# Optimization experiments

Hardware: AMD Instinct MI355X
Metric: run time of the kernel (lower is better)

## Reference

```python
import jax, jax.numpy as jnp
import numpy as np

B, H, S, D = 1, 16, 4096, 64
TEMPERATURE = 8.0          # sqrt(d_k)
WINDOW_SIZE = 256
HALF_WINDOW = WINDOW_SIZE // 2
NEG_INF = -1000000000.0


def setup_inputs() -> dict:
    key = jax.random.key(0)
    kq, kk, kv = jax.random.split(key, 3)
    q = jax.random.normal(kq, (B, H, S, D), dtype=jnp.float32)
    k = jax.random.normal(kk, (B, H, S, D), dtype=jnp.float32)
    v = jax.random.normal(kv, (B, H, S, D), dtype=jnp.float32)
    return {"q": q, "k": k, "v": v}


def reference(q, k, v):
    # q,k,v: [B,H,S,D]
    seq = q.shape[2]
    attn = jnp.einsum('bhqd,bhkd->bhqk', q, k) / TEMPERATURE  # [B,H,S,S]
    if seq > WINDOW_SIZE:
        idx = jnp.arange(seq)
        # torch loop: row i allows columns [i-half, i+half] inclusive
        win = jnp.abs(idx[:, None] - idx[None, :]) <= HALF_WINDOW  # [S,S]
        attn = jnp.where(win[None, None, :, :], attn, NEG_INF)
    attn = jax.nn.softmax(attn, axis=-1)  # dropout p=0 -> identity
    out = jnp.einsum('bhqk,bhkd->bhqd', attn, v)
    return (out, attn)
```

## Files before the change

### kernel.cpp

```cpp
#include <hip/hip_runtime.h>
#include <hip/hip_bf16.h>


typedef short bf16x8 __attribute__((ext_vector_type(8)));
typedef float f32x4  __attribute__((ext_vector_type(4)));
typedef unsigned int u32;
typedef unsigned short u16;

namespace {
constexpr int S = 4096, H = 16, Dh = 64, TRB = 64, HW = 128, NCH = 5;
constexpr int KP  = 72;
constexpr int NTILE = H * (S / TRB);
}

__device__ __forceinline__ u16 f2bf(float x) {
    u32 u = __float_as_uint(x);
    return (u16)((u + 0x7fffu + ((u >> 16) & 1u)) >> 16);
}
__device__ __forceinline__ float bf2f(u16 h) {
    return __uint_as_float(((u32)h) << 16);
}

__device__ __forceinline__ void bar_lds() {
    asm volatile("s_waitcnt lgkmcnt(0)" ::: "memory");
    __builtin_amdgcn_s_barrier();
    asm volatile("" ::: "memory");
}

__global__ __launch_bounds__(256)
void zfill(float* __restrict__ attn)
{
    constexpr size_t NF4     = (size_t)H * S * S / 4;
    constexpr size_t PER_BLK = NF4 / 256;
    f32x4* dst = (f32x4*)attn + (size_t)blockIdx.x * PER_BLK;
    const f32x4 z4 = {0.f, 0.f, 0.f, 0.f};
    for (size_t i = threadIdx.x; i < PER_BLK; i += 1024) {
        dst[i]       = z4;
        dst[i + 256] = z4;
        dst[i + 512] = z4;
        dst[i + 768] = z4;
    }
}

__global__ __launch_bounds__(256, 4)
void wattn(const float* __restrict__ q, const float* __restrict__ k,
           const float* __restrict__ v, float* __restrict__ out,
           float* __restrict__ attn)
{
    __shared__ __align__(16) u16 hbuf[4 * 64 * KP];
    __shared__ float inv_row[TRB];
    u16* kh_ = hbuf;
    u16* kl_ = hbuf + 64 * KP;
    u16* vt_ = hbuf + 2 * 64 * KP;
    u16* pc_ = hbuf + 3 * 64 * KP;

    const int tid  = threadIdx.x;
    const int wave = tid >> 6, lane = tid & 63;
    const int g = lane >> 4, m = lane & 15;

    int bx = blockIdx.x;
    bx = (bx & 7) * (NTILE / 8) + (bx >> 3);
    const int h  = bx >> 6;
    const int r0 = (bx & 63) * TRB;
    const int c0 = max(0, r0 - HW);
    const int c1 = min(S - 1, r0 + TRB - 1 + HW);
    const int c0q = c0 >> 2;

    const float* qp = q + ((size_t)h * S + r0) * Dh;
    const float* kp = k + (size_t)h * S * Dh;
    const float* vp = v + (size_t)h * S * Dh;
    float* arow = attn + ((size_t)h * S + r0) * S;

    bf16x8 aqh[2], aql[2];
    #pragma unroll
    for (int ks = 0; ks < 2; ++ks) {
        const float* qsrc = qp + (wave * 16 + m) * Dh + ks * 32 + g * 8;
        float4 t0 = *(const float4*)(qsrc);
        float4 t1 = *(const float4*)(qsrc + 4);
        float xs[8] = {t0.x, t0.y, t0.z, t0.w, t1.x, t1.y, t1.z, t1.w};
        #pragma unroll
        for (int i = 0; i < 8; ++i) {
            u16 hi = f2bf(xs[i]);
            aqh[ks][i] = (short)hi;
            aql[ks][i] = (short)f2bf(xs[i] - bf2f(hi));
        }
    }

    const int kcol = tid >> 2, kd = (tid & 3) * 16;
    const int vj = tid & 63, vd = (tid >> 6) * 16;

    float4 rk[4], rv[4];
    {
        const float* src = kp + (size_t)min(c0 + kcol, S - 1) * Dh + kd;
        #pragma unroll
        for (int i4 = 0; i4 < 4; ++i4) rk[i4] = *(const float4*)(src + i4 * 4);
    }
    {
        const float* src = vp + (size_t)min(c0 + vj, S - 1) * Dh + vd;
        #pragma unroll
        for (int i4 = 0; i4 < 4; ++i4) rv[i4] = *(const float4*)(src + i4 * 4);
    }

    float rs[4] = {0.f, 0.f, 0.f, 0.f};
    f32x4 oacc[4] = {{0.f,0.f,0.f,0.f},{0.f,0.f,0.f,0.f},
                     {0.f,0.f,0.f,0.f},{0.f,0.f,0.f,0.f}};

    for (int cc = 0; cc < NCH; ++cc) {
        if (cc) bar_lds();
        {
            u16* dh = kh_ + kcol * KP + kd;
            u16* dl = kl_ + kcol * KP + kd;
            #pragma unroll
            for (int i4 = 0; i4 < 4; ++i4) {
                float xs[4] = {rk[i4].x, rk[i4].y, rk[i4].z, rk[i4].w};
                #pragma unroll
                for (int i = 0; i < 4; ++i) {
                    u16 hi = f2bf(xs[i]);
                    dh[i4 * 4 + i] = hi;
                    dl[i4 * 4 + i] = f2bf(xs[i] - bf2f(hi));
                }
            }
        }
        #pragma unroll
        for (int i4 = 0; i4 < 4; ++i4) {
            float xs[4] = {rv[i4].x, rv[i4].y, rv[i4].z, rv[i4].w};
            #pragma unroll
            for (int i = 0; i < 4; ++i)
                vt_[(vd + i4 * 4 + i) * KP + vj] = f2bf(xs[i]);
        }
        if (cc + 1 < NCH) {
            const float* srck = kp + (size_t)min(c0 + (cc + 1) * 64 + kcol, S - 1) * Dh + kd;
            const float* srcv = vp + (size_t)min(c0 + (cc + 1) * 64 + vj,   S - 1) * Dh + vd;
            #pragma unroll
            for (int i4 = 0; i4 < 4; ++i4) {
                rk[i4] = *(const float4*)(srck + i4 * 4);
                rv[i4] = *(const float4*)(srcv + i4 * 4);
            }
        }
        bar_lds();
        f32x4 acc[4] = {{0.f,0.f,0.f,0.f},{0.f,0.f,0.f,0.f},
                        {0.f,0.f,0.f,0.f},{0.f,0.f,0.f,0.f}};
        #pragma unroll
        for (int ci = 0; ci < 4; ++ci) {
            #pragma unroll
            for (int ks = 0; ks < 2; ++ks) {
                bf16x8 bh = *(const bf16x8*)(kh_ + (ci * 16 + m) * KP + ks * 32 + g * 8);
                bf16x8 bl = *(const bf16x8*)(kl_ + (ci * 16 + m) * KP + ks * 32 + g * 8);
                acc[ci] = __builtin_amdgcn_mfma_f32_16x16x32_bf16(aqh[ks], bh, acc[ci], 0, 0, 0);
                acc[ci] = __builtin_amdgcn_mfma_f32_16x16x32_bf16(aql[ks], bh, acc[ci], 0, 0, 0);
                acc[ci] = __builtin_amdgcn_mfma_f32_16x16x32_bf16(aqh[ks], bl, acc[ci], 0, 0, 0);
            }
        }
        #pragma unroll
        for (int ci = 0; ci < 4; ++ci) {
            const int colg = c0 + cc * 64 + ci * 16 + m;
            #pragma unroll
            for (int w = 0; w < 4; ++w) {
                const int row = r0 + wave * 16 + g * 4 + w;
                const float l = acc[ci][w] * 0.125f;
                const bool ok = (colg >= row - HW) && (colg <= row + HW) && (colg <= c1);
                const float ev = ok ? __expf(l) : 0.f;
                rs[w] += ev;
                pc_[(wave * 16 + g * 4 + w) * KP + ci * 16 + m] = f2bf(ev);
            }
        }
        bar_lds();
        {
            const int br = tid >> 2, bc = tid & 3;
            #pragma unroll
            for (int it = 0; it < 4; ++it) {
                const int c = bc + 4 * it;
                const int col4 = c0q + cc * 16 + c;
                if (col4 < S / 4) {
                    ushort4 hh = *(const ushort4*)(pc_ + br * KP + c * 4);
                    float4 val;
                    val.x = bf2f(hh.x); val.y = bf2f(hh.y);
                    val.z = bf2f(hh.z); val.w = bf2f(hh.w);
                    ((float4*)(arow + (size_t)br * S))[col4] = val;
                }
            }
        }
        #pragma unroll
        for (int di = 0; di < 4; ++di) {
            #pragma unroll
            for (int ks = 0; ks < 2; ++ks) {
                bf16x8 ap = *(const bf16x8*)(pc_ + (wave * 16 + m) * KP + ks * 32 + g * 8);
                bf16x8 bv = *(const bf16x8*)(vt_ + (di * 16 + m) * KP + ks * 32 + g * 8);
                oacc[di] = __builtin_amdgcn_mfma_f32_16x16x32_bf16(ap, bv, oacc[di], 0, 0, 0);
            }
        }
    }

    #pragma unroll
    for (int off = 1; off < 16; off <<= 1) {
        #pragma unroll
        for (int w = 0; w < 4; ++w) rs[w] += __shfl_xor(rs[w], off, 64);
    }
    float invw[4];
    #pragma unroll
    for (int w = 0; w < 4; ++w) invw[w] = 1.0f / rs[w];
    if (m == 0) {
        #pragma unroll
        for (int w = 0; w < 4; ++w) inv_row[wave * 16 + g * 4 + w] = invw[w];
    }

    {
        float* ob = out + ((size_t)h * S + r0 + wave * 16) * Dh;
        #pragma unroll
        for (int di = 0; di < 4; ++di)
            #pragma unroll
            for (int w = 0; w < 4; ++w)
                ob[(g * 4 + w) * Dh + di * 16 + m] = oacc[di][w] * invw[w];
    }

    asm volatile("s_waitcnt vmcnt(0)" ::: "memory");
    bar_lds();
    #pragma unroll 4
    for (int it = 0; it < 20; ++it) {
        const int idx = tid + 256 * it;
        const int r = idx / 80;
        const int c = idx - r * 80;
        const int col4 = c0q + c;
        if (col4 < S / 4) {
            float4* p = (float4*)(arow + (size_t)r * S) + col4;
            float4 t = *p;
            const float iv = inv_row[r];
            t.x *= iv; t.y *= iv; t.z *= iv; t.w *= iv;
            *p = t;
        }
    }
}

extern "C" void kernel_launch(void* const* d_in, const int* in_sizes, int n_in,
                              void* d_out, int out_size, void* d_ws, size_t ws_size,
                              hipStream_t stream) {
    const float* q = (const float*)d_in[0];
    const float* k = (const float*)d_in[1];
    const float* v = (const float*)d_in[2];
    float* out  = (float*)d_out;
    float* attn = out + (size_t)H * S * Dh;
    zfill<<<dim3(256), dim3(256), 0, stream>>>(attn);
    wattn<<<dim3(NTILE), dim3(256), 0, stream>>>(q, k, v, out, attn);
}
```

Measured before the change: 1.132 ms.

## Buffer full probability band in LDS and write normalized attn once

Instead of writing unnormalized probabilities to global memory per chunk and then reading them back to rescale, the kernel keeps the whole 64x320 bf16 probability band in LDS and writes normalized values once at the end. This removes a global read-modify-write pass over the band. The zero-fill kernel now launches more blocks and uses nontemporal stores, and the output stores are nontemporal too. The larger LDS footprint lowers the occupancy target from 4 to 2 blocks per CU.

Result: no change. 1.122 ms (-0.9%).

```diff
diff --git a/kernel.cpp b/kernel.cpp
--- a/kernel.cpp
+++ b/kernel.cpp
@@ -10,6 +10,7 @@
 namespace {
 constexpr int S = 4096, H = 16, Dh = 64, TRB = 64, HW = 128, NCH = 5;
 constexpr int KP  = 72;
+constexpr int PBW = 328;
 constexpr int NTILE = H * (S / TRB);
 }
 
@@ -30,29 +31,30 @@
 __global__ __launch_bounds__(256)
 void zfill(float* __restrict__ attn)
 {
-    constexpr size_t NF4     = (size_t)H * S * S / 4;
-    constexpr size_t PER_BLK = NF4 / 256;
-    f32x4* dst = (f32x4*)attn + (size_t)blockIdx.x * PER_BLK;
+    constexpr size_t NF4 = (size_t)H * S * S / 4;
+    constexpr size_t PER = NF4 / 2048;
+    f32x4* dst = (f32x4*)attn + (size_t)blockIdx.x * PER;
     const f32x4 z4 = {0.f, 0.f, 0.f, 0.f};
-    for (size_t i = threadIdx.x; i < PER_BLK; i += 1024) {
-        dst[i]       = z4;
-        dst[i + 256] = z4;
-        dst[i + 512] = z4;
-        dst[i + 768] = z4;
-    }
-}
-
-__global__ __launch_bounds__(256, 4)
+    for (size_t i = threadIdx.x; i < PER; i += 1024) {
+        __builtin_nontemporal_store(z4, dst + i);
+        __builtin_nontemporal_store(z4, dst + i + 256);
+        __builtin_nontemporal_store(z4, dst + i + 512);
+        __builtin_nontemporal_store(z4, dst + i + 768);
+    }
+}
+
+__global__ __launch_bounds__(256, 2)
 void wattn(const float* __restrict__ q, const float* __restrict__ k,
            const float* __restrict__ v, float* __restrict__ out,
            float* __restrict__ attn)
 {
-    __shared__ __align__(16) u16 hbuf[4 * 64 * KP];
+    __shared__ __align__(16) u16 hbuf[3 * 64 * KP];
+    __shared__ __align__(16) u16 pbuf[64 * PBW];
     __shared__ float inv_row[TRB];
     u16* kh_ = hbuf;
     u16* kl_ = hbuf + 64 * KP;
     u16* vt_ = hbuf + 2 * 64 * KP;
-    u16* pc_ = hbuf + 3 * 64 * KP;
+    u16* pb_ = pbuf;
 
     const int tid  = threadIdx.x;
     const int wave = tid >> 6, lane = tid & 63;
@@ -161,30 +163,14 @@
                 const bool ok = (colg >= row - HW) && (colg <= row + HW) && (colg <= c1);
                 const float ev = ok ? __expf(l) : 0.f;
                 rs[w] += ev;
-                pc_[(wave * 16 + g * 4 + w) * KP + ci * 16 + m] = f2bf(ev);
-            }
-        }
-        bar_lds();
-        {
-            const int br = tid >> 2, bc = tid & 3;
-            #pragma unroll
-            for (int it = 0; it < 4; ++it) {
-                const int c = bc + 4 * it;
-                const int col4 = c0q + cc * 16 + c;
-                if (col4 < S / 4) {
-                    ushort4 hh = *(const ushort4*)(pc_ + br * KP + c * 4);
-                    float4 val;
-                    val.x = bf2f(hh.x); val.y = bf2f(hh.y);
-                    val.z = bf2f(hh.z); val.w = bf2f(hh.w);
-                    ((float4*)(arow + (size_t)br * S))[col4] = val;
-                }
+                pb_[(wave * 16 + g * 4 + w) * PBW + cc * 64 + ci * 16 + m] = f2bf(ev);
             }
         }
         #pragma unroll
         for (int di = 0; di < 4; ++di) {
             #pragma unroll
             for (int ks = 0; ks < 2; ++ks) {
-                bf16x8 ap = *(const bf16x8*)(pc_ + (wave * 16 + m) * KP + ks * 32 + g * 8);
+                bf16x8 ap = *(const bf16x8*)(pb_ + (wave * 16 + m) * PBW + cc * 64 + ks * 32 + g * 8);
                 bf16x8 bv = *(const bf16x8*)(vt_ + (di * 16 + m) * KP + ks * 32 + g * 8);
                 oacc[di] = __builtin_amdgcn_mfma_f32_16x16x32_bf16(ap, bv, oacc[di], 0, 0, 0);
             }
@@ -210,23 +196,24 @@
         for (int di = 0; di < 4; ++di)
             #pragma unroll
             for (int w = 0; w < 4; ++w)
-                ob[(g * 4 + w) * Dh + di * 16 + m] = oacc[di][w] * invw[w];
-    }
-
-    asm volatile("s_waitcnt vmcnt(0)" ::: "memory");
+                __builtin_nontemporal_store(oacc[di][w] * invw[w],
+                                            ob + (g * 4 + w) * Dh + di * 16 + m);
+    }
+
     bar_lds();
-    #pragma unroll 4
+
     for (int it = 0; it < 20; ++it) {
         const int idx = tid + 256 * it;
         const int r = idx / 80;
         const int c = idx - r * 80;
         const int col4 = c0q + c;
         if (col4 < S / 4) {
-            float4* p = (float4*)(arow + (size_t)r * S) + col4;
-            float4 t = *p;
-            const float iv = inv_row[r];
-            t.x *= iv; t.y *= iv; t.z *= iv; t.w *= iv;
-            *p = t;
+            ushort4 hh = *(const ushort4*)(pb_ + r * PBW + c * 4);
+            const float inv = inv_row[r];
+            f32x4 val;
+            val[0] = bf2f(hh.x) * inv; val[1] = bf2f(hh.y) * inv;
+            val[2] = bf2f(hh.z) * inv; val[3] = bf2f(hh.w) * inv;
+            __builtin_nontemporal_store(val, (f32x4*)(arow + (size_t)r * S) + col4);
         }
     }
 }
@@ -239,6 +226,6 @@
     const float* v = (const float*)d_in[2];
     float* out  = (float*)d_out;
     float* attn = out + (size_t)H * S * Dh;
-    zfill<<<dim3(256), dim3(256), 0, stream>>>(attn);
+    zfill<<<dim3(2048), dim3(256), 0, stream>>>(attn);
     wattn<<<dim3(NTILE), dim3(256), 0, stream>>>(q, k, v, out, attn);
 }
```
